# Performance work log

Hardware: AMD Instinct MI355X
Metric: run time of the kernel (lower is better)

Reference implementation:

```python
import jax, jax.numpy as jnp
import numpy as np

BLADES = ['', '1', '2', '3', '12', '13', '23', '123']
GEOM_DEF = (3, 0, 0)  # e1,e2,e3 all square to +1
M = len(BLADES)  # multivector length = 8


def _square_vector(idx):
    l = [0]
    for sq, cnt in zip([1, -1, 0], GEOM_DEF):
        l += [sq] * cnt
    return l[idx]


def _ga_multiply_get_index(index_1, index_2):
    l1 = [int(i) for i in index_1]
    l2 = [int(i) for i in index_2]
    s = 1
    i1, i2, length_l1 = 0, 0, len(l1)
    out_l = []
    while i1 < len(l1) and i2 < len(l2):
        if l1[i1] == l2[i2]:
            if (length_l1 - 1) % 2 != 0:
                s *= -1
            s *= _square_vector(l1[i1])
            length_l1 -= 1
            i1 += 1
            i2 += 1
        elif l1[i1] > l2[i2]:
            if length_l1 % 2 != 0:
                s *= -1
            out_l.append(l2[i2])
            i2 += 1
        else:
            out_l.append(l1[i1])
            length_l1 -= 1
            i1 += 1
    out_l += l1[i1:] + l2[i2:]
    return s, ''.join(str(i) for i in out_l)


def _combine_tensor():
    # C[k, i, j] = s where blade_i * blade_j = s * blade_k
    pos = {e: p for p, e in enumerate(BLADES)}
    C = np.zeros((M, M, M), dtype=np.float32)
    for i in range(M):
        for j in range(M):
            s, idx = _ga_multiply_get_index(BLADES[i], BLADES[j])
            C[pos[idx], i, j] = float(s)
    return C

_C = jnp.asarray(_combine_tensor())  # [8, 8, 8]


def setup_inputs() -> dict:
    B, DIN, DOUT = 2048, 2048, 2048  # per-blade batch, in features, out features per blade
    U = M * DOUT  # Dense units = 16384
    key = jax.random.key(0)
    k1, k2, k3 = jax.random.split(key, 3)
    x = jax.random.normal(k1, (M * B, DIN), dtype=jnp.float32)
    W = jax.random.normal(k2, (DIN, U), dtype=jnp.float32) * 0.02
    bias = jax.random.normal(k3, (U,), dtype=jnp.float32) * 0.02
    return {"input_tensor": x, "W": W, "bias": bias}


def reference(input_tensor, W, bias):
    eightB, DIN = input_tensor.shape
    B = eightB // M
    U = W.shape[1]
    D = U // M
    # Dense (no bias inside): [8B, DIN] @ [DIN, U] -> [8B, U]
    y = input_tensor @ W
    # split axis 0 into 8 blades, axis 1 into 8 blade-components: [i=8, B, j=8, D]
    y = y.reshape(M, B, M, D)
    # BiasLayer applied to blade-0 output only (shape [B, U] = [B, 8, D])
    y = y.at[0].add(bias.reshape(M, D)[None, :, :])
    # sign-weighted accumulate: out[k] = sum_{i,j} C[k,i,j] * y[i,:,j,:]
    out = jnp.einsum('kij,ibjd->kbd', _C, y)
    # Concatenate along axis 0 -> [8B, D]
    return out.reshape(M * B, D)
```

## Files before the change

kernel.cpp:

```cpp
#include <hip/hip_runtime.h>
#include <hip/hip_bf16.h>
#include <stdint.h>


#define BATCH 2048
#define DIN 2048
#define DD 2048
#define K2 4096
#define R2R 4096

typedef __attribute__((ext_vector_type(8))) __bf16 bf16x8;
typedef __attribute__((ext_vector_type(4))) float f32x4;
typedef __attribute__((ext_vector_type(4))) unsigned int u32x4;

#define NEG 0x80008000u

__device__ __forceinline__ unsigned short f2bf(float f) {
  unsigned int u = __float_as_uint(f);
  u = (u + 0x7FFFu + ((u >> 16) & 1u)) >> 16;
  return (unsigned short)u;
}

__device__ __forceinline__ u32x4 pack8(const float* s) {
  u32x4 p;
#pragma unroll
  for (int w = 0; w < 4; ++w)
    p[w] = (unsigned)f2bf(s[2 * w]) | ((unsigned)f2bf(s[2 * w + 1]) << 16);
  return p;
}

__device__ __forceinline__ void gl_lds16(const void* g, void* l) {
  __builtin_amdgcn_global_load_lds((__attribute__((address_space(1))) void*)g,
                                   (__attribute__((address_space(3))) void*)l,
                                   16, 0, 0);
}

union FragU {
  u32x4 u;
  bf16x8 v;
};

__global__ void pack_x(const float* __restrict__ x,
                       unsigned short* __restrict__ Ar,
                       unsigned short* __restrict__ Ai) {
  const int b = blockIdx.x;
  const int l0 = threadIdx.x * 8;
  float v[8][8];
#pragma unroll
  for (int i = 0; i < 8; ++i) {
    const float4* p = (const float4*)&x[((size_t)i * BATCH + b) * DIN + l0];
    float4 a = p[0], c = p[1];
    v[i][0] = a.x; v[i][1] = a.y; v[i][2] = a.z; v[i][3] = a.w;
    v[i][4] = c.x; v[i][5] = c.y; v[i][6] = c.z; v[i][7] = c.w;
  }
  const size_t r0 = (size_t)(2 * b) * K2;
  const size_t r1 = (size_t)(2 * b + 1) * K2;
  float t[8];
#pragma unroll
  for (int e = 0; e < 8; ++e) t[e] = 0.5f * (v[0][e] + v[3][e]);
  *(u32x4*)&Ar[r0 + l0] = pack8(t);
#pragma unroll
  for (int e = 0; e < 8; ++e) t[e] = 0.5f * (v[1][e] - v[5][e]);
  *(u32x4*)&Ar[r0 + DIN + l0] = pack8(t);
#pragma unroll
  for (int e = 0; e < 8; ++e) t[e] = 0.5f * (v[1][e] + v[5][e]);
  *(u32x4*)&Ar[r1 + l0] = pack8(t);
#pragma unroll
  for (int e = 0; e < 8; ++e) t[e] = 0.5f * (v[0][e] - v[3][e]);
  *(u32x4*)&Ar[r1 + DIN + l0] = pack8(t);
#pragma unroll
  for (int e = 0; e < 8; ++e) t[e] = 0.5f * (v[7][e] + v[4][e]);
  *(u32x4*)&Ai[r0 + l0] = pack8(t);
#pragma unroll
  for (int e = 0; e < 8; ++e) t[e] = 0.5f * (v[6][e] - v[2][e]);
  *(u32x4*)&Ai[r0 + DIN + l0] = pack8(t);
#pragma unroll
  for (int e = 0; e < 8; ++e) t[e] = 0.5f * (v[6][e] + v[2][e]);
  *(u32x4*)&Ai[r1 + l0] = pack8(t);
#pragma unroll
  for (int e = 0; e < 8; ++e) t[e] = 0.5f * (v[7][e] - v[4][e]);
  *(u32x4*)&Ai[r1 + DIN + l0] = pack8(t);
}

__constant__ int c_pw[4][2] = {{0, 3}, {1, 5}, {7, 4}, {6, 2}};

__global__ void pack_w(const float* __restrict__ W,
                       unsigned short* __restrict__ Br,
                       unsigned short* __restrict__ Bi) {
  __shared__ float ts[64][65], td[64][65];
  const int z = blockIdx.z;
  const int p0 = c_pw[z][0], p1 = c_pw[z][1];
  unsigned short* dst = (z < 2) ? Br : Bi;
  const int rs = z & 1;
  const int rd = rs ^ 1;
  const int d0 = blockIdx.x * 64;
  const int l0 = blockIdx.y * 64;
  const int tid = threadIdx.x;
  {
    const int row = tid >> 4;
    const int col = (tid & 15) * 4;
#pragma unroll
    for (int j = 0; j < 4; ++j) {
      const size_t base = (size_t)(l0 + row + j * 16) * (8 * DD);
      float4 a = *(const float4*)&W[base + (size_t)p0 * DD + d0 + col];
      float4 b = *(const float4*)&W[base + (size_t)p1 * DD + d0 + col];
      ts[row + j * 16][col + 0] = a.x + b.x;
      ts[row + j * 16][col + 1] = a.y + b.y;
      ts[row + j * 16][col + 2] = a.z + b.z;
      ts[row + j * 16][col + 3] = a.w + b.w;
      td[row + j * 16][col + 0] = a.x - b.x;
      td[row + j * 16][col + 1] = a.y - b.y;
      td[row + j * 16][col + 2] = a.z - b.z;
      td[row + j * 16][col + 3] = a.w - b.w;
    }
  }
  __syncthreads();
  {
    const int rc = (tid & 7) * 8;
    int c = tid >> 3;
#pragma unroll
    for (int h = 0; h < 2; ++h, c += 32) {
      float s[8], dl[8];
#pragma unroll
      for (int w = 0; w < 8; ++w) {
        s[w] = ts[rc + w][c];
        dl[w] = td[rc + w][c];
      }
      *(u32x4*)&dst[(size_t)(d0 + c) * K2 + rs * DIN + l0 + rc] = pack8(s);
      *(u32x4*)&dst[(size_t)(DD + d0 + c) * K2 + rd * DIN + l0 + rc] = pack8(dl);
    }
  }
}

__global__ __launch_bounds__(256, 2) void cplx_gemm(
    const unsigned short* __restrict__ Ar, const unsigned short* __restrict__ Ai,
    const unsigned short* __restrict__ Br, const unsigned short* __restrict__ Bi,
    const float* __restrict__ bias, float* __restrict__ out) {
  __shared__ u32x4 ldsAr[1024], ldsAi[1024], ldsBr[1024], ldsBi[1024];

  const int tid = threadIdx.x;
  const int tn = blockIdx.x;
  const int tm = blockIdx.y;
  const int wid = tid >> 6;
  const int lane = tid & 63;
  const int wr = wid & 1;
  const int wc = wid >> 1;
  const int lrow = lane & 15;
  const int q4 = lane >> 4;
  const int l7 = lane & 7;
  const u32x4 nmask = {NEG, NEG, NEG, NEG};

  f32x4 accR[4][4] = {};
  f32x4 accI[4][4] = {};

  const size_t arow0 = (size_t)tm * 128;
  const int d0 = tn * 64;

  for (int k0 = 0; k0 < K2; k0 += 64) {
#pragma unroll
    for (int t = 0; t < 4; ++t) {
      const int L = (t * 4 + wid) * 64 + lane;
      const int m = L >> 3;
      const int c = (L & 7) ^ (m & 7);
      const size_t ao = (arow0 + m) * K2 + (k0 + c * 8);
      gl_lds16(Ar + ao, &ldsAr[(t * 4 + wid) * 64]);
      gl_lds16(Ai + ao, &ldsAi[(t * 4 + wid) * 64]);
      const size_t bo = ((size_t)((m >> 6) * DD + d0 + (m & 63))) * K2 + (k0 + c * 8);
      gl_lds16(Br + bo, &ldsBr[(t * 4 + wid) * 64]);
      gl_lds16(Bi + bo, &ldsBi[(t * 4 + wid) * 64]);
    }
    __syncthreads();

#pragma unroll
    for (int kk = 0; kk < 2; ++kk) {
      const int p = (kk * 4 + q4) ^ l7;
      FragU arf[4], aif[4], brf[4], bif[4];
#pragma unroll
      for (int mt = 0; mt < 4; ++mt) {
        const int ml = wr * 64 + mt * 16 + lrow;
        arf[mt].u = ldsAr[ml * 8 + p];
        aif[mt].u = ldsAi[ml * 8 + p];
      }
#pragma unroll
      for (int nt = 0; nt < 4; ++nt) {
        const int nl = (nt >> 1) * 64 + wc * 32 + (nt & 1) * 16 + lrow;
        brf[nt].u = ldsBr[nl * 8 + p];
        bif[nt].u = ldsBi[nl * 8 + p];
      }
#pragma unroll
      for (int mt = 0; mt < 4; ++mt) {
        FragU ain;
        ain.u = aif[mt].u ^ nmask;
#pragma unroll
        for (int nt = 0; nt < 4; ++nt) {
          accR[mt][nt] = __builtin_amdgcn_mfma_f32_16x16x32_bf16(
              arf[mt].v, brf[nt].v, accR[mt][nt], 0, 0, 0);
          accR[mt][nt] = __builtin_amdgcn_mfma_f32_16x16x32_bf16(
              ain.v, bif[nt].v, accR[mt][nt], 0, 0, 0);
          accI[mt][nt] = __builtin_amdgcn_mfma_f32_16x16x32_bf16(
              arf[mt].v, bif[nt].v, accI[mt][nt], 0, 0, 0);
          accI[mt][nt] = __builtin_amdgcn_mfma_f32_16x16x32_bf16(
              aif[mt].v, brf[nt].v, accI[mt][nt], 0, 0, 0);
        }
      }
    }
    __syncthreads();
  }

  const size_t ks = (size_t)BATCH * DD;
#pragma unroll
  for (int ntd = 0; ntd < 2; ++ntd) {
    const int d = d0 + wc * 32 + ntd * 16 + lrow;
    float bv[8];
#pragma unroll
    for (int k = 0; k < 8; ++k) bv[k] = bias[k * DD + d];
#pragma unroll
    for (int mt = 0; mt < 4; ++mt) {
      const int rowbase = tm * 128 + wr * 64 + mt * 16 + q4 * 4;
      const f32x4 R0 = accR[mt][ntd], R1 = accR[mt][2 + ntd];
      const f32x4 I0 = accI[mt][ntd], I1 = accI[mt][2 + ntd];
#pragma unroll
      for (int j = 0; j < 2; ++j) {
        const int b = (rowbase >> 1) + j;
        const float y00r = R0[2 * j], y10r = R0[2 * j + 1];
        const float y01r = R1[2 * j], y11r = R1[2 * j + 1];
        const float y00i = I0[2 * j], y10i = I0[2 * j + 1];
        const float y01i = I1[2 * j], y11i = I1[2 * j + 1];
        float* o = out + (size_t)b * DD + d;
        o[0]          = (y00r + y11r) + bv[0];
        o[ks]         = (y01r + y10r) + bv[1];
        o[2 * ks]     = (y10i - y01i) + bv[2];
        o[3 * ks]     = (y00r - y11r) + bv[3];
        o[4 * ks]     = (y00i - y11i) + bv[4];
        o[5 * ks]     = (y10r - y01r) + bv[5];
        o[6 * ks]     = (y01i + y10i) + bv[6];
        o[7 * ks]     = (y00i + y11i) + bv[7];
      }
    }
  }
}

extern "C" void kernel_launch(void* const* d_in, const int* in_sizes, int n_in,
                              void* d_out, int out_size, void* d_ws,
                              size_t ws_size, hipStream_t stream) {
  const float* x = (const float*)d_in[0];
  const float* W = (const float*)d_in[1];
  const float* bias = (const float*)d_in[2];
  float* out = (float*)d_out;

  unsigned short* Arp = (unsigned short*)d_ws;
  unsigned short* Aip = Arp + (size_t)R2R * K2;
  unsigned short* Brp = Aip + (size_t)R2R * K2;
  unsigned short* Bip = Brp + (size_t)(2 * DD) * K2;

  pack_x<<<BATCH, 256, 0, stream>>>(x, Arp, Aip);
  pack_w<<<dim3(DD / 64, DIN / 64, 4), 256, 0, stream>>>(W, Brp, Bip);
  cplx_gemm<<<dim3(DD / 64, R2R / 128), 256, 0, stream>>>(Arp, Aip, Brp, Bip,
                                                          bias, out);
}
```

Baseline: 724.2 us.

## Pipeline complex GEMM with 4-stage LDS ring, 512 threads and block swizzle

Rewrites the complex bf16 GEMM main loop as a 4-buffer LDS ring. Each step loads a 32-wide K slice, and waits with vmcnt keep three slices in flight, so global-to-LDS loads overlap MFMA work. The block grows to 512 threads (8 waves, each with a 4x2 fragment tile), uses a new XOR-swizzled LDS layout, and remaps block IDs so neighbouring blocks share tiles in cache. It raises wave priority around the MFMA section and uses explicit barriers. The cost is more LDS per block and a few wasted prefetch loads at the wrap-around.

```diff
diff --git a/kernel.cpp b/kernel.cpp
--- a/kernel.cpp
+++ b/kernel.cpp
@@ -8,6 +8,7 @@
 #define DD 2048
 #define K2 4096
 #define R2R 4096
+#define NSLICE 128
 
 typedef __attribute__((ext_vector_type(8))) __bf16 bf16x8;
 typedef __attribute__((ext_vector_type(4))) float f32x4;
@@ -79,7 +80,7 @@
   *(u32x4*)&Ai[r1 + l0] = pack8(t);
 #pragma unroll
   for (int e = 0; e < 8; ++e) t[e] = 0.5f * (v[7][e] - v[4][e]);
-  *(u32x4*)&Ai[r1 + DIN + l0] = pack8(t);
+  *(u32x4*)&Ai[r1 + l0 + DIN] = pack8(t);
 }
 
 __constant__ int c_pw[4][2] = {{0, 3}, {1, 5}, {7, 4}, {6, 2}};
@@ -132,110 +133,150 @@
   }
 }
 
-__global__ __launch_bounds__(256, 2) void cplx_gemm(
+__global__ __launch_bounds__(512, 2) void cplx_gemm(
     const unsigned short* __restrict__ Ar, const unsigned short* __restrict__ Ai,
     const unsigned short* __restrict__ Br, const unsigned short* __restrict__ Bi,
     const float* __restrict__ bias, float* __restrict__ out) {
-  __shared__ u32x4 ldsAr[1024], ldsAi[1024], ldsBr[1024], ldsBi[1024];
+  __shared__ u32x4 lds[4][4][512];
 
   const int tid = threadIdx.x;
-  const int tn = blockIdx.x;
-  const int tm = blockIdx.y;
   const int wid = tid >> 6;
   const int lane = tid & 63;
-  const int wr = wid & 1;
-  const int wc = wid >> 1;
   const int lrow = lane & 15;
   const int q4 = lane >> 4;
-  const int l7 = lane & 7;
   const u32x4 nmask = {NEG, NEG, NEG, NEG};
 
-  f32x4 accR[4][4] = {};
-  f32x4 accI[4][4] = {};
-
+  int flat = blockIdx.y * 32 + blockIdx.x;
+  flat = (flat & 7) * 128 + (flat >> 3);
+  const int tn = flat & 31;
+  const int tm = flat >> 5;
+  const int d0 = tn * 64;
   const size_t arow0 = (size_t)tm * 128;
-  const int d0 = tn * 64;
-
-  for (int k0 = 0; k0 < K2; k0 += 64) {
-#pragma unroll
-    for (int t = 0; t < 4; ++t) {
-      const int L = (t * 4 + wid) * 64 + lane;
-      const int m = L >> 3;
-      const int c = (L & 7) ^ (m & 7);
-      const size_t ao = (arow0 + m) * K2 + (k0 + c * 8);
-      gl_lds16(Ar + ao, &ldsAr[(t * 4 + wid) * 64]);
-      gl_lds16(Ai + ao, &ldsAi[(t * 4 + wid) * 64]);
-      const size_t bo = ((size_t)((m >> 6) * DD + d0 + (m & 63))) * K2 + (k0 + c * 8);
-      gl_lds16(Br + bo, &ldsBr[(t * 4 + wid) * 64]);
-      gl_lds16(Bi + bo, &ldsBi[(t * 4 + wid) * 64]);
-    }
-    __syncthreads();
-
-#pragma unroll
-    for (int kk = 0; kk < 2; ++kk) {
-      const int p = (kk * 4 + q4) ^ l7;
-      FragU arf[4], aif[4], brf[4], bif[4];
-#pragma unroll
-      for (int mt = 0; mt < 4; ++mt) {
-        const int ml = wr * 64 + mt * 16 + lrow;
-        arf[mt].u = ldsAr[ml * 8 + p];
-        aif[mt].u = ldsAi[ml * 8 + p];
-      }
-#pragma unroll
-      for (int nt = 0; nt < 4; ++nt) {
-        const int nl = (nt >> 1) * 64 + wc * 32 + (nt & 1) * 16 + lrow;
-        brf[nt].u = ldsBr[nl * 8 + p];
-        bif[nt].u = ldsBi[nl * 8 + p];
-      }
-#pragma unroll
-      for (int mt = 0; mt < 4; ++mt) {
-        FragU ain;
-        ain.u = aif[mt].u ^ nmask;
-#pragma unroll
-        for (int nt = 0; nt < 4; ++nt) {
-          accR[mt][nt] = __builtin_amdgcn_mfma_f32_16x16x32_bf16(
-              arf[mt].v, brf[nt].v, accR[mt][nt], 0, 0, 0);
-          accR[mt][nt] = __builtin_amdgcn_mfma_f32_16x16x32_bf16(
-              ain.v, bif[nt].v, accR[mt][nt], 0, 0, 0);
-          accI[mt][nt] = __builtin_amdgcn_mfma_f32_16x16x32_bf16(
-              arf[mt].v, bif[nt].v, accI[mt][nt], 0, 0, 0);
-          accI[mt][nt] = __builtin_amdgcn_mfma_f32_16x16x32_bf16(
-              aif[mt].v, brf[nt].v, accI[mt][nt], 0, 0, 0);
-        }
-      }
-    }
-    __syncthreads();
-  }
+
+  const int sline = tid >> 3;
+  const int scl = (tid & 7) ^ (sline & 7);
+  const int srow = 2 * sline + (scl >> 2);
+  const int skc = scl & 3;
+  const unsigned short* gAr = Ar + (arow0 + srow) * (size_t)K2 + skc * 8;
+  const unsigned short* gAi = Ai + (arow0 + srow) * (size_t)K2 + skc * 8;
+  const size_t offB =
+      ((size_t)((srow >> 6) * DD + d0 + (srow & 63))) * K2 + skc * 8;
+  const unsigned short* gBr = Br + offB;
+  const unsigned short* gBi = Bi + offB;
+
+  const int wrow = (wid >> 2) * 64;
+  const int wc = wid & 3;
+  int slotA[4], slotB[2];
+#pragma unroll
+  for (int mt = 0; mt < 4; ++mt) {
+    const int r = wrow + mt * 16 + lrow;
+    const int ln = r >> 1;
+    const int cl = (r & 1) * 4 + q4;
+    slotA[mt] = ln * 8 + (cl ^ (ln & 7));
+  }
+#pragma unroll
+  for (int nt = 0; nt < 2; ++nt) {
+    const int r = nt * 64 + wc * 16 + lrow;
+    const int ln = r >> 1;
+    const int cl = (r & 1) * 4 + q4;
+    slotB[nt] = ln * 8 + (cl ^ (ln & 7));
+  }
+
+  f32x4 accR[4][2] = {};
+  f32x4 accI[4][2] = {};
+
+#define STAGE(B3, S3)                                      \
+  {                                                        \
+    const size_t ko = (size_t)(S3) * 32;                   \
+    gl_lds16(gAr + ko, &lds[B3][0][wid * 64]);             \
+    gl_lds16(gAi + ko, &lds[B3][1][wid * 64]);             \
+    gl_lds16(gBr + ko, &lds[B3][2][wid * 64]);             \
+    gl_lds16(gBi + ko, &lds[B3][3][wid * 64]);             \
+  }
+
+#define SLICE(BB)                                                         \
+  {                                                                       \
+    FragU arf[4], aif[4], brf[2], bif[2];                                 \
+    _Pragma("unroll") for (int mt = 0; mt < 4; ++mt) {                    \
+      arf[mt].u = lds[BB][0][slotA[mt]];                                  \
+      aif[mt].u = lds[BB][1][slotA[mt]];                                  \
+    }                                                                     \
+    _Pragma("unroll") for (int nt = 0; nt < 2; ++nt) {                    \
+      brf[nt].u = lds[BB][2][slotB[nt]];                                  \
+      bif[nt].u = lds[BB][3][slotB[nt]];                                  \
+    }                                                                     \
+    asm volatile("s_waitcnt lgkmcnt(0)" ::: "memory");                    \
+    __builtin_amdgcn_s_barrier();                                         \
+    __builtin_amdgcn_sched_barrier(0);                                    \
+    __builtin_amdgcn_s_setprio(1);                                        \
+    _Pragma("unroll") for (int mt = 0; mt < 4; ++mt) {                    \
+      FragU ain;                                                          \
+      ain.u = aif[mt].u ^ nmask;                                          \
+      _Pragma("unroll") for (int nt = 0; nt < 2; ++nt) {                  \
+        accR[mt][nt] = __builtin_amdgcn_mfma_f32_16x16x32_bf16(           \
+            arf[mt].v, brf[nt].v, accR[mt][nt], 0, 0, 0);                 \
+        accR[mt][nt] = __builtin_amdgcn_mfma_f32_16x16x32_bf16(           \
+            ain.v, bif[nt].v, accR[mt][nt], 0, 0, 0);                     \
+        accI[mt][nt] = __builtin_amdgcn_mfma_f32_16x16x32_bf16(           \
+            arf[mt].v, bif[nt].v, accI[mt][nt], 0, 0, 0);                 \
+        accI[mt][nt] = __builtin_amdgcn_mfma_f32_16x16x32_bf16(           \
+            aif[mt].v, brf[nt].v, accI[mt][nt], 0, 0, 0);                 \
+      }                                                                   \
+    }                                                                     \
+    __builtin_amdgcn_s_setprio(0);                                        \
+  }
+
+  STAGE(0, 0)
+  STAGE(1, 1)
+  STAGE(2, 2)
+
+  int s3 = 3;
+#define ITER(OFF)                                        \
+  {                                                      \
+    STAGE((OFF + 3) & 3, s3)                             \
+    if (++s3 == NSLICE) s3 = 0;                          \
+    asm volatile("s_waitcnt vmcnt(12)" ::: "memory");    \
+    __builtin_amdgcn_s_barrier();                        \
+    __builtin_amdgcn_sched_barrier(0);                   \
+    SLICE(OFF)                                           \
+  }
+
+  for (int s0 = 0; s0 < NSLICE; s0 += 4) {
+    ITER(0)
+    ITER(1)
+    ITER(2)
+    ITER(3)
+  }
+#undef ITER
+#undef SLICE
+#undef STAGE
 
   const size_t ks = (size_t)BATCH * DD;
-#pragma unroll
-  for (int ntd = 0; ntd < 2; ++ntd) {
-    const int d = d0 + wc * 32 + ntd * 16 + lrow;
-    float bv[8];
-#pragma unroll
-    for (int k = 0; k < 8; ++k) bv[k] = bias[k * DD + d];
-#pragma unroll
-    for (int mt = 0; mt < 4; ++mt) {
-      const int rowbase = tm * 128 + wr * 64 + mt * 16 + q4 * 4;
-      const f32x4 R0 = accR[mt][ntd], R1 = accR[mt][2 + ntd];
-      const f32x4 I0 = accI[mt][ntd], I1 = accI[mt][2 + ntd];
-#pragma unroll
-      for (int j = 0; j < 2; ++j) {
-        const int b = (rowbase >> 1) + j;
-        const float y00r = R0[2 * j], y10r = R0[2 * j + 1];
-        const float y01r = R1[2 * j], y11r = R1[2 * j + 1];
-        const float y00i = I0[2 * j], y10i = I0[2 * j + 1];
-        const float y01i = I1[2 * j], y11i = I1[2 * j + 1];
-        float* o = out + (size_t)b * DD + d;
-        o[0]          = (y00r + y11r) + bv[0];
-        o[ks]         = (y01r + y10r) + bv[1];
-        o[2 * ks]     = (y10i - y01i) + bv[2];
-        o[3 * ks]     = (y00r - y11r) + bv[3];
-        o[4 * ks]     = (y00i - y11i) + bv[4];
-        o[5 * ks]     = (y10r - y01r) + bv[5];
-        o[6 * ks]     = (y01i + y10i) + bv[6];
-        o[7 * ks]     = (y00i + y11i) + bv[7];
-      }
+  const int d = d0 + wc * 16 + lrow;
+  float bv[8];
+#pragma unroll
+  for (int k = 0; k < 8; ++k) bv[k] = bias[k * DD + d];
+#pragma unroll
+  for (int mt = 0; mt < 4; ++mt) {
+    const int rowbase = tm * 128 + wrow + mt * 16 + q4 * 4;
+    const f32x4 R0 = accR[mt][0], R1 = accR[mt][1];
+    const f32x4 I0 = accI[mt][0], I1 = accI[mt][1];
+#pragma unroll
+    for (int j = 0; j < 2; ++j) {
+      const int b = (rowbase >> 1) + j;
+      const float y00r = R0[2 * j], y10r = R0[2 * j + 1];
+      const float y01r = R1[2 * j], y11r = R1[2 * j + 1];
+      const float y00i = I0[2 * j], y10i = I0[2 * j + 1];
+      const float y01i = I1[2 * j], y11i = I1[2 * j + 1];
+      float* o = out + (size_t)b * DD + d;
+      o[0]      = (y00r + y11r) + bv[0];
+      o[ks]     = (y01r + y10r) + bv[1];
+      o[2 * ks] = (y10i - y01i) + bv[2];
+      o[3 * ks] = (y00r - y11r) + bv[3];
+      o[4 * ks] = (y00i - y11i) + bv[4];
+      o[5 * ks] = (y10r - y01r) + bv[5];
+      o[6 * ks] = (y01i + y10i) + bv[6];
+      o[7 * ks] = (y00i + y11i) + bv[7];
     }
   }
 }
@@ -255,6 +296,5 @@
 
   pack_x<<<BATCH, 256, 0, stream>>>(x, Arp, Aip);
   pack_w<<<dim3(DD / 64, DIN / 64, 4), 256, 0, stream>>>(W, Brp, Bip);
-  cplx_gemm<<<dim3(DD / 64, R2R / 128), 256, 0, stream>>>(Arp, Aip, Brp, Bip,
-                                                          bias, out);
-}
+  cplx_gemm<<<dim3(32, 32), 512, 0, stream>>>(Arp, Aip, Brp, Bip, bias, out);
+}
```

Result: slower. 844.1 us (+16.5%).

## Double-buffer LDS tiles in complex GEMM with K-step 32 and interleaved real/imag

Applied to the files above, without the earlier changes.

Restructures the complex bf16 GEMM main loop into a two-stage LDS ping-pong. The next K-slice is loaded from global memory while MFMAs run on the current one, replacing the load-sync-compute-sync loop. Real and imaginary halves now share one LDS buffer, addressed by offsetting into the contiguous workspace, and the K step drops from 64 to 32 with precomputed offsets, swizzled slots and s_setprio around the MFMA block. The trade-off is hand-placed waitcnt and barrier logic, where any miscount breaks correctness, and the same total LDS footprint split across two buffers.

```diff
diff --git a/kernel.cpp b/kernel.cpp
--- a/kernel.cpp
+++ b/kernel.cpp
@@ -8,6 +8,7 @@
 #define DD 2048
 #define K2 4096
 #define R2R 4096
+#define NT 128
 
 typedef __attribute__((ext_vector_type(8))) __bf16 bf16x8;
 typedef __attribute__((ext_vector_type(4))) float f32x4;
@@ -133,79 +134,116 @@
 }
 
 __global__ __launch_bounds__(256, 2) void cplx_gemm(
-    const unsigned short* __restrict__ Ar, const unsigned short* __restrict__ Ai,
-    const unsigned short* __restrict__ Br, const unsigned short* __restrict__ Bi,
+    const unsigned short* __restrict__ Ar, const unsigned short* __restrict__ Br,
     const float* __restrict__ bias, float* __restrict__ out) {
-  __shared__ u32x4 ldsAr[1024], ldsAi[1024], ldsBr[1024], ldsBi[1024];
+  __shared__ u32x4 AC[2][1024];
+  __shared__ u32x4 BC[2][1024];
 
   const int tid = threadIdx.x;
+  const int wid = tid >> 6;
+  const int lane = tid & 63;
+  const int lrow = lane & 15;
+  const int q4 = lane >> 4;
+  const int wr = wid & 1;
+  const int wc = wid >> 1;
+  const u32x4 nmask = {NEG, NEG, NEG, NEG};
+
   const int tn = blockIdx.x;
   const int tm = blockIdx.y;
-  const int wid = tid >> 6;
-  const int lane = tid & 63;
-  const int wr = wid & 1;
-  const int wc = wid >> 1;
-  const int lrow = lane & 15;
-  const int q4 = lane >> 4;
-  const int l7 = lane & 7;
-  const u32x4 nmask = {NEG, NEG, NEG, NEG};
+  const int d0 = tn * 64;
+  const size_t arow0 = (size_t)tm * 128;
+
+  unsigned int aoff[4], boff[4];
+#pragma unroll
+  for (int t = 0; t < 4; ++t) {
+    const int L = t * 256 + tid;
+    const int m = L >> 3;
+    const int c = (L & 7) ^ (m & 7);
+    const unsigned int imag = (c >> 2) ? (unsigned int)R2R * K2 : 0u;
+    aoff[t] = imag + (unsigned int)(arow0 + m) * K2 + (c & 3) * 8;
+    const unsigned int brow = (m >> 6) * DD + d0 + (m & 63);
+    boff[t] = imag + brow * (unsigned int)K2 + (c & 3) * 8;
+  }
+
+  int slotA[4], slotB[4];
+#pragma unroll
+  for (int mt = 0; mt < 4; ++mt) {
+    const int r = wr * 64 + mt * 16 + lrow;
+    slotA[mt] = r * 8 + (q4 ^ (r & 7));
+  }
+#pragma unroll
+  for (int nt = 0; nt < 4; ++nt) {
+    const int r = (nt >> 1) * 64 + wc * 32 + (nt & 1) * 16 + lrow;
+    slotB[nt] = r * 8 + (q4 ^ (r & 7));
+  }
 
   f32x4 accR[4][4] = {};
   f32x4 accI[4][4] = {};
 
-  const size_t arow0 = (size_t)tm * 128;
-  const int d0 = tn * 64;
-
-  for (int k0 = 0; k0 < K2; k0 += 64) {
-#pragma unroll
-    for (int t = 0; t < 4; ++t) {
-      const int L = (t * 4 + wid) * 64 + lane;
-      const int m = L >> 3;
-      const int c = (L & 7) ^ (m & 7);
-      const size_t ao = (arow0 + m) * K2 + (k0 + c * 8);
-      gl_lds16(Ar + ao, &ldsAr[(t * 4 + wid) * 64]);
-      gl_lds16(Ai + ao, &ldsAi[(t * 4 + wid) * 64]);
-      const size_t bo = ((size_t)((m >> 6) * DD + d0 + (m & 63))) * K2 + (k0 + c * 8);
-      gl_lds16(Br + bo, &ldsBr[(t * 4 + wid) * 64]);
-      gl_lds16(Bi + bo, &ldsBi[(t * 4 + wid) * 64]);
-    }
-    __syncthreads();
-
-#pragma unroll
-    for (int kk = 0; kk < 2; ++kk) {
-      const int p = (kk * 4 + q4) ^ l7;
-      FragU arf[4], aif[4], brf[4], bif[4];
-#pragma unroll
-      for (int mt = 0; mt < 4; ++mt) {
-        const int ml = wr * 64 + mt * 16 + lrow;
-        arf[mt].u = ldsAr[ml * 8 + p];
-        aif[mt].u = ldsAi[ml * 8 + p];
-      }
-#pragma unroll
-      for (int nt = 0; nt < 4; ++nt) {
-        const int nl = (nt >> 1) * 64 + wc * 32 + (nt & 1) * 16 + lrow;
-        brf[nt].u = ldsBr[nl * 8 + p];
-        bif[nt].u = ldsBi[nl * 8 + p];
-      }
-#pragma unroll
-      for (int mt = 0; mt < 4; ++mt) {
-        FragU ain;
-        ain.u = aif[mt].u ^ nmask;
-#pragma unroll
-        for (int nt = 0; nt < 4; ++nt) {
-          accR[mt][nt] = __builtin_amdgcn_mfma_f32_16x16x32_bf16(
-              arf[mt].v, brf[nt].v, accR[mt][nt], 0, 0, 0);
-          accR[mt][nt] = __builtin_amdgcn_mfma_f32_16x16x32_bf16(
-              ain.v, bif[nt].v, accR[mt][nt], 0, 0, 0);
-          accI[mt][nt] = __builtin_amdgcn_mfma_f32_16x16x32_bf16(
-              arf[mt].v, bif[nt].v, accI[mt][nt], 0, 0, 0);
-          accI[mt][nt] = __builtin_amdgcn_mfma_f32_16x16x32_bf16(
-              aif[mt].v, brf[nt].v, accI[mt][nt], 0, 0, 0);
-        }
-      }
-    }
-    __syncthreads();
-  }
+#define STAGE(BUF, KT)                                          \
+  {                                                             \
+    const unsigned int ko = (unsigned int)(KT) * 32u;           \
+    _Pragma("unroll") for (int t = 0; t < 4; ++t) {             \
+      gl_lds16(Ar + aoff[t] + ko, &AC[BUF][t * 256 + wid * 64]);\
+      gl_lds16(Br + boff[t] + ko, &BC[BUF][t * 256 + wid * 64]);\
+    }                                                           \
+  }
+
+#define COMPUTE(BUF)                                                      \
+  {                                                                       \
+    FragU arf[4], aif[4], brf[4], bif[4];                                 \
+    _Pragma("unroll") for (int mt = 0; mt < 4; ++mt) {                    \
+      arf[mt].u = AC[BUF][slotA[mt]];                                     \
+      aif[mt].u = AC[BUF][slotA[mt] ^ 4];                                 \
+    }                                                                     \
+    _Pragma("unroll") for (int nt = 0; nt < 4; ++nt) {                    \
+      brf[nt].u = BC[BUF][slotB[nt]];                                     \
+      bif[nt].u = BC[BUF][slotB[nt] ^ 4];                                 \
+    }                                                                     \
+    asm volatile("s_waitcnt lgkmcnt(0)" ::: "memory");                    \
+    __builtin_amdgcn_s_barrier();  \
+    __builtin_amdgcn_sched_barrier(0);                                    \
+    __builtin_amdgcn_s_setprio(1);                                        \
+    _Pragma("unroll") for (int mt = 0; mt < 4; ++mt) {                    \
+      FragU ain;                                                          \
+      ain.u = aif[mt].u ^ nmask;                                          \
+      _Pragma("unroll") for (int nt = 0; nt < 4; ++nt) {                  \
+        accR[mt][nt] = __builtin_amdgcn_mfma_f32_16x16x32_bf16(           \
+            arf[mt].v, brf[nt].v, accR[mt][nt], 0, 0, 0);                 \
+        accR[mt][nt] = __builtin_amdgcn_mfma_f32_16x16x32_bf16(           \
+            ain.v, bif[nt].v, accR[mt][nt], 0, 0, 0);                     \
+        accI[mt][nt] = __builtin_amdgcn_mfma_f32_16x16x32_bf16(           \
+            arf[mt].v, bif[nt].v, accI[mt][nt], 0, 0, 0);                 \
+        accI[mt][nt] = __builtin_amdgcn_mfma_f32_16x16x32_bf16(           \
+            aif[mt].v, brf[nt].v, accI[mt][nt], 0, 0, 0);                 \
+      }                                                                   \
+    }                                                                     \
+    __builtin_amdgcn_s_setprio(0);                                        \
+  }
+
+#define ITER(BUF, KT)                                     \
+  {                                                       \
+    STAGE(BUF ^ 1, KT)                                    \
+    asm volatile("s_waitcnt vmcnt(8)" ::: "memory");      \
+    __builtin_amdgcn_s_barrier();                         \
+    __builtin_amdgcn_sched_barrier(0);                    \
+    COMPUTE(BUF)                                          \
+  }
+
+  STAGE(0, 0)
+  int kt = 1;
+  for (int pair = 0; pair < 63; ++pair) {
+    ITER(0, kt) ++kt;
+    ITER(1, kt) ++kt;
+  }
+  ITER(0, 127)
+  asm volatile("s_waitcnt vmcnt(0)" ::: "memory");
+  __builtin_amdgcn_s_barrier();
+  __builtin_amdgcn_sched_barrier(0);
+  COMPUTE(1)
+#undef ITER
+#undef COMPUTE
+#undef STAGE
 
   const size_t ks = (size_t)BATCH * DD;
 #pragma unroll
@@ -227,14 +265,14 @@
         const float y00i = I0[2 * j], y10i = I0[2 * j + 1];
         const float y01i = I1[2 * j], y11i = I1[2 * j + 1];
         float* o = out + (size_t)b * DD + d;
-        o[0]          = (y00r + y11r) + bv[0];
-        o[ks]         = (y01r + y10r) + bv[1];
-        o[2 * ks]     = (y10i - y01i) + bv[2];
-        o[3 * ks]     = (y00r - y11r) + bv[3];
-        o[4 * ks]     = (y00i - y11i) + bv[4];
-        o[5 * ks]     = (y10r - y01r) + bv[5];
-        o[6 * ks]     = (y01i + y10i) + bv[6];
-        o[7 * ks]     = (y00i + y11i) + bv[7];
+        o[0]      = (y00r + y11r) + bv[0];
+        o[ks]     = (y01r + y10r) + bv[1];
+        o[2 * ks] = (y10i - y01i) + bv[2];
+        o[3 * ks] = (y00r - y11r) + bv[3];
+        o[4 * ks] = (y00i - y11i) + bv[4];
+        o[5 * ks] = (y10r - y01r) + bv[5];
+        o[6 * ks] = (y01i + y10i) + bv[6];
+        o[7 * ks] = (y00i + y11i) + bv[7];
       }
     }
   }
@@ -255,6 +293,5 @@
 
   pack_x<<<BATCH, 256, 0, stream>>>(x, Arp, Aip);
   pack_w<<<dim3(DD / 64, DIN / 64, 4), 256, 0, stream>>>(W, Brp, Bip);
-  cplx_gemm<<<dim3(DD / 64, R2R / 128), 256, 0, stream>>>(Arp, Aip, Brp, Bip,
-                                                          bias, out);
-}
+  cplx_gemm<<<dim3(32, 32), 256, 0, stream>>>(Arp, Brp, bias, out);
+}
```

Result: slower. 778.4 us (+7.5%).
